# Optimization experiments

Hardware: AMD Instinct MI355X
Metric: run time of the kernel (lower is better)

## Reference

```python
import jax, jax.numpy as jnp
import numpy as np

N, E = 10000, 160000          # nodes, edges
MUL = 128                     # channel multiplicity of 0e and 1o blocks
NSP = 10                      # node_attrs (species one-hot) dim
NRAD = 8                      # edge_feats radial basis dim
SILU_C = 1.6790               # e3nn normalize2mom constant for SiLU
AVG_NEIGH = 16.0
SQ3 = np.sqrt(3.0).astype(np.float32)


def setup_inputs() -> dict:
    key = jax.random.key(0)
    ks = jax.random.split(key, 14)
    d = {}
    d["node_feats"] = jax.random.normal(ks[0], (N, 4 * MUL), jnp.float32)   # [N, 128 + 128*3]
    d["node_attrs"] = jax.random.normal(ks[1], (N, NSP), jnp.float32)
    d["edge_feats"] = jax.random.normal(ks[2], (E, NRAD), jnp.float32)
    d["edge_attrs"] = jax.random.normal(ks[3], (E, 4), jnp.float32)          # [0e | 1o]
    d["edge_index"] = jax.random.randint(ks[4], (2, E), 0, N, jnp.int32)
    # e3nn internal weights are standard normal; normalization applied in forward
    d["lin1_ws"] = jax.random.normal(ks[5], (MUL, MUL), jnp.float32)
    d["lin1_wv"] = jax.random.normal(ks[6], (MUL, MUL), jnp.float32)
    d["fc_w0"] = jax.random.normal(ks[7], (NRAD, 64), jnp.float32)
    d["fc_w1"] = jax.random.normal(ks[8], (64, 64), jnp.float32)
    d["fc_w2"] = jax.random.normal(ks[9], (64, 4 * MUL), jnp.float32)        # tp.weight_numel = 512
    d["lin2_ws"] = jax.random.normal(ks[10], (2 * MUL, MUL), jnp.float32)    # 256x0e -> 128x0e
    d["lin2_wv"] = jax.random.normal(ks[11], (2 * MUL, MUL), jnp.float32)    # 256x1o -> 128x1o
    d["sc_ws"] = jax.random.normal(ks[12], (MUL, NSP, MUL), jnp.float32)
    d["sc_wv"] = jax.random.normal(ks[13], (MUL, NSP, MUL), jnp.float32)
    return d


def _fc(ef, w0, w1, w2):
    # e3nn FullyConnectedNet: x @ W / sqrt(fan_in), normalize2mom-scaled SiLU between layers
    h = SILU_C * jax.nn.silu(ef @ w0 / np.float32(np.sqrt(NRAD)))
    h = SILU_C * jax.nn.silu(h @ w1 / np.float32(8.0))
    return h @ w2 / np.float32(8.0)


def reference(node_feats, node_attrs, edge_feats, edge_attrs, edge_index,
              lin1_ws, lin1_wv, fc_w0, fc_w1, fc_w2,
              lin2_ws, lin2_wv, sc_ws, sc_wv):
    x_s = node_feats[:, :MUL]                       # [N, 128] scalar block
    x_v = node_feats[:, MUL:].reshape(N, MUL, 3)    # [N, 128, 3] vector block

    # self-connection: FullyConnectedTensorProduct with 10x0e attrs; path weight 1/sqrt(mul1*mul2)
    sc_norm = np.float32(1.0 / np.sqrt(MUL * NSP))
    sc_s = jnp.einsum('nu,nv,uvw->nw', x_s, node_attrs, sc_ws) * sc_norm
    sc_v = jnp.einsum('nuc,nv,uvw->nwc', x_v, node_attrs, sc_wv) * sc_norm

    # linear_1 (per-irrep channel mixing, fan_in = 128)
    l1 = np.float32(1.0 / np.sqrt(MUL))
    y_s = (x_s @ lin1_ws) * l1
    y_v = jnp.einsum('nuc,uw->nwc', x_v, lin1_wv) * l1

    src = edge_index[1]
    dst = edge_index[0]
    xs_e = y_s[src]                                 # [E, 128]
    xv_e = y_v[src]                                 # [E, 128, 3]
    a_s = edge_attrs[:, :1]                         # [E, 1]
    a_v = edge_attrs[:, 1:]                         # [E, 3]

    w = _fc(edge_feats, fc_w0, fc_w1, fc_w2)        # [E, 512]
    w_ss, w_sv, w_vs, w_vv = jnp.split(w, 4, axis=1)  # instruction order in source

    # 'uvu' weighted tensor product with e3nn component/element normalization:
    # net coefficient per path works out to 1 except 1o x 1o -> 0e which is 1/sqrt(3)
    mid_s0 = w_ss * xs_e * a_s                                          # 0e*0e->0e
    mid_s1 = w_vv * jnp.einsum('euc,ec->eu', xv_e, a_v) / SQ3           # 1o*1o->0e
    mid_v2 = (w_sv * xs_e)[:, :, None] * a_v[:, None, :]                # 0e*1o->1o
    mid_v3 = w_vs[:, :, None] * xv_e * a_s[:, :, None]                  # 1o*0e->1o

    inv = np.float32(1.0 / np.sqrt(AVG_NEIGH))
    s = jax.ops.segment_sum(jnp.concatenate([mid_s0, mid_s1], axis=1), dst, num_segments=N) * inv  # [N, 256]
    v = jax.ops.segment_sum(jnp.concatenate([mid_v2, mid_v3], axis=1), dst, num_segments=N) * inv  # [N, 256, 3]

    # linear_2 (fan_in = 256)
    l2 = np.float32(1.0 / np.sqrt(2 * MUL))
    out_s = (s @ lin2_ws) * l2 + sc_s
    out_v = jnp.einsum('nuc,uw->nwc', v, lin2_wv) * l2 + sc_v

    return jnp.concatenate([out_s, out_v.reshape(N, 3 * MUL)], axis=1)   # [N, 512]
```

## Files before the change

### kernel.cpp

```cpp
#include <hip/hip_runtime.h>
#include <hip/hip_bf16.h>
#include <math.h>

#define N_NODES 10000
#define N_EDGES 160000
#define S_BLK 79
#define V_BLK 235

typedef __attribute__((ext_vector_type(8))) short short8x;
typedef __attribute__((ext_vector_type(4))) float floatx4;
typedef __attribute__((ext_vector_type(4))) unsigned int uint4x;
typedef __attribute__((ext_vector_type(2))) unsigned int uint2x;

union S8 { short8x v; unsigned short u[8]; uint4 q; };
union U2 { uint2x v; unsigned short us[4]; };

__device__ __forceinline__ unsigned short f2bf(float x) {
    unsigned int u = __float_as_uint(x);
    return (unsigned short)((u + 0x7fffu + ((u >> 16) & 1u)) >> 16);
}
__device__ __forceinline__ float bf2f(unsigned short u) {
    return __uint_as_float(((unsigned)u) << 16);
}
__device__ __forceinline__ float silu_c(float x) {
    return 1.679f * x / (1.0f + __expf(-x));
}

__global__ __launch_bounds__(256) void pack_all_kernel(
    const float* __restrict__ sc_ws, const float* __restrict__ lin2_ws,
    const float* __restrict__ sc_wv, const float* __restrict__ lin2_wv,
    const float* __restrict__ fc_w2, const float* __restrict__ fc_w1,
    const float* __restrict__ lin1_ws, const float* __restrict__ lin1_wv,
    unsigned short* __restrict__ b_pre, unsigned short* __restrict__ w2a,
    unsigned short* __restrict__ w1a, unsigned short* __restrict__ b_lin)
{
    const int bid = blockIdx.x;
    const int t = threadIdx.x;
    if (bid < 192) {
        int id = bid * 256 + t;
        int mat = id / 24576;
        int slot = id - mat * 24576;
        int ks = slot >> 9;
        int rr = slot & 511;
        int lane = rr & 63;
        int quad = lane >> 4;
        int n = ((rr >> 6) << 4) + (lane & 15);
        const float* sc  = mat ? sc_wv  : sc_ws;
        const float* lin = mat ? lin2_wv : lin2_ws;
        S8 pk;
        #pragma unroll
        for (int j = 0; j < 8; j++) {
            int k = ks * 32 + quad * 8 + j;
            float w;
            if (k < 1280) {
                int u = k & 127, v = k >> 7;
                w = sc[(u * 10 + v) * 128 + n];
            } else {
                w = lin[(k - 1280) * 128 + n];
            }
            pk.u[j] = f2bf(w);
        }
        *(uint4*)(b_pre + (size_t)id * 8) = pk.q;
    } else if (bid < 208) {
        int id = (bid - 192) * 256 + t;
        int lane = id & 63;
        int mfg = (id >> 6) & 31;
        int ks = id >> 11;
        int col = mfg * 16 + (lane & 15);
        int k0 = ks * 32 + (lane >> 4) * 8;
        S8 pk;
        #pragma unroll
        for (int j = 0; j < 8; j++)
            pk.u[j] = f2bf(fc_w2[(k0 + j) * 512 + col] * 0.125f);
        *(uint4*)(w2a + (size_t)id * 8) = pk.q;
    } else if (bid < 210) {
        int id = (bid - 208) * 256 + t;
        int lane = id & 63;
        int mf = (id >> 6) & 3;
        int ks = id >> 8;
        int m = mf * 16 + (lane & 15);
        int k0 = ks * 32 + (lane >> 4) * 8;
        S8 pk;
        #pragma unroll
        for (int j = 0; j < 8; j++)
            pk.u[j] = f2bf(fc_w1[(k0 + j) * 64 + m] * 0.125f);
        *(uint4*)(w1a + (size_t)id * 8) = pk.q;
    } else {
        int id = (bid - 210) * 256 + t;
        int mat = id >> 11;
        int slot = id & 2047;
        int ks = slot >> 9;
        int rr = slot & 511;
        int nf = rr >> 6;
        int lane = rr & 63;
        int n = nf * 16 + (lane & 15);
        int k0 = ks * 32 + (lane >> 4) * 8;
        const float* w = mat ? lin1_wv : lin1_ws;
        const float l1 = 0.0883883476483f;
        S8 pk;
        #pragma unroll
        for (int j = 0; j < 8; j++)
            pk.u[j] = f2bf(w[(k0 + j) * 128 + n] * l1);
        *(uint4*)(b_lin + (size_t)id * 8) = pk.q;
    }
}

__global__ __launch_bounds__(256) void node_lin1_mfma(
    const float* __restrict__ node_feats,
    const unsigned short* __restrict__ b_lin,
    unsigned short* __restrict__ y_pk,
    unsigned short* __restrict__ xvP16)
{
    __shared__ __align__(16) unsigned char smem[32768];
    short8x* Al = (short8x*)smem;
    unsigned short* Yt = (unsigned short*)smem;

    const int blk = blockIdx.x;
    const int t = threadIdx.x;
    const int base = blk * 32;
    const int lane = t & 63;
    const int wv = t >> 6;
    const int m15 = lane & 15;
    const int k0q = (lane >> 4) * 8;

    #pragma unroll
    for (int it = 0; it < 8; it++) {
        int g = wv * 8 + it;
        int af = g >> 2;
        int ks = g & 3;
        int m = af * 16 + m15;
        int comp = m >> 5;
        int nloc = m & 31;
        int node = base + nloc;
        int valid = (node < N_NODES);
        if (!valid) node = N_NODES - 1;
        int k0 = ks * 32 + k0q;
        const float* row = node_feats + (size_t)node * 512;
        S8 pk;
        if (comp == 0) {
            float4 a = *(const float4*)&row[k0];
            float4 b = *(const float4*)&row[k0 + 4];
            pk.u[0] = f2bf(a.x); pk.u[1] = f2bf(a.y); pk.u[2] = f2bf(a.z); pk.u[3] = f2bf(a.w);
            pk.u[4] = f2bf(b.x); pk.u[5] = f2bf(b.y); pk.u[6] = f2bf(b.z); pk.u[7] = f2bf(b.w);
        } else {
            int c = comp - 1;
            #pragma unroll
            for (int j = 0; j < 8; j++)
                pk.u[j] = f2bf(row[128 + (k0 + j) * 3 + c]);
            if (valid)
                *(uint4*)&xvP16[((size_t)node * 3 + c) * 128 + k0] = pk.q;
        }
        Al[(ks * 8 + af) * 64 + lane] = pk.v;
    }
    __syncthreads();

    floatx4 c[8][2];
    #pragma unroll
    for (int af = 0; af < 8; af++) {
        c[af][0] = (floatx4){0.f, 0.f, 0.f, 0.f};
        c[af][1] = (floatx4){0.f, 0.f, 0.f, 0.f};
    }

    const uint4* bq = (const uint4*)b_lin;
    #pragma unroll
    for (int ks = 0; ks < 4; ks++) {
        S8 bs0, bs1, bv0, bv1;
        bs0.q = bq[       ks*512 + (wv*2+0)*64 + lane];
        bs1.q = bq[       ks*512 + (wv*2+1)*64 + lane];
        bv0.q = bq[2048 + ks*512 + (wv*2+0)*64 + lane];
        bv1.q = bq[2048 + ks*512 + (wv*2+1)*64 + lane];
        #pragma unroll
        for (int af = 0; af < 8; af++) {
            short8x a = Al[(ks*8 + af)*64 + lane];
            if (af < 2) {
                c[af][0] = __builtin_amdgcn_mfma_f32_16x16x32_bf16(a, bs0.v, c[af][0], 0, 0, 0);
                c[af][1] = __builtin_amdgcn_mfma_f32_16x16x32_bf16(a, bs1.v, c[af][1], 0, 0, 0);
            } else {
                c[af][0] = __builtin_amdgcn_mfma_f32_16x16x32_bf16(a, bv0.v, c[af][0], 0, 0, 0);
                c[af][1] = __builtin_amdgcn_mfma_f32_16x16x32_bf16(a, bv1.v, c[af][1], 0, 0, 0);
            }
        }
    }
    __syncthreads();

    {
        const int rq = (lane >> 4) * 4;
        #pragma unroll
        for (int af = 0; af < 8; af++) {
            #pragma unroll
            for (int nf = 0; nf < 2; nf++) {
                int u = wv * 32 + nf * 16 + m15;
                #pragma unroll
                for (int i = 0; i < 4; i++) {
                    int m = af * 16 + rq + i;
                    int comp = m >> 5, nloc = m & 31;
                    Yt[(nloc * 128 + u) * 4 + comp] = f2bf(c[af][nf][i]);
                }
            }
        }
    }
    __syncthreads();
    {
        unsigned short* dst = y_pk + (size_t)base * 512;
        int nrem = N_NODES - base;
        #pragma unroll
        for (int it = 0; it < 8; it++) {
            int idx = it * 256 + t;
            if ((idx >> 6) < nrem)
                *(uint4*)(dst + (size_t)idx * 8) = *(const uint4*)&Yt[idx * 8];
        }
    }
}

__global__ __launch_bounds__(256) void hist_kernel(const int* __restrict__ edge_index,
                                                   int* __restrict__ deg) {
    int e = blockIdx.x * 256 + threadIdx.x;
    if (e < N_EDGES) atomicAdd(&deg[edge_index[e]], 1);
}

__global__ __launch_bounds__(1024) void scan_kernel(const int* __restrict__ deg,
                                                    int* __restrict__ row_start,
                                                    int* __restrict__ cursor) {
    __shared__ int wsum[16];
    __shared__ int carry_s;
    const int t = threadIdx.x;
    const int lane = t & 63, w = t >> 6;
    if (t == 0) carry_s = 0;
    __syncthreads();
    for (int chunk = 0; chunk < 10; chunk++) {
        int idx = chunk * 1024 + t;
        int v = (idx < N_NODES) ? deg[idx] : 0;
        int x = v;
        #pragma unroll
        for (int off = 1; off < 64; off <<= 1) {
            int yv = __shfl_up(x, off, 64);
            if (lane >= off) x += yv;
        }
        if (lane == 63) wsum[w] = x;
        __syncthreads();
        int wpre = 0;
        for (int i = 0; i < w; i++) wpre += wsum[i];
        int incl = x + wpre + carry_s;
        int excl = incl - v;
        if (idx < N_NODES) { row_start[idx] = excl; cursor[idx] = excl; }
        __syncthreads();
        if (t == 1023) carry_s = incl;
        __syncthreads();
    }
    if (t == 0) row_start[N_NODES] = carry_s;
}

__global__ __launch_bounds__(256) void scatter_kernel(const int* __restrict__ edge_index,
                                                      const float* __restrict__ edge_attrs,
                                                      int* __restrict__ cursor,
                                                      int* __restrict__ edge_list,
                                                      int* __restrict__ srcs,
                                                      float* __restrict__ ea_sorted) {
    int e = blockIdx.x * 256 + threadIdx.x;
    if (e < N_EDGES) {
        int pos = atomicAdd(&cursor[edge_index[e]], 1);
        edge_list[pos] = e;
        srcs[pos] = edge_index[N_EDGES + e];
        float4 ea = *(const float4*)(edge_attrs + (size_t)e * 4);
        *(float4*)(ea_sorted + (size_t)pos * 4) = ea;
    }
}

__global__ __launch_bounds__(256) void edge_w_mfma(
    const float* __restrict__ edge_feats,
    const int* __restrict__ edge_list,
    const float* __restrict__ fc_w0,
    const unsigned short* __restrict__ w1a,
    const unsigned short* __restrict__ w2a,
    unsigned short* __restrict__ w_pk)
{
    __shared__ __align__(16) unsigned char smem[26368];
    float* ef = (float*)smem;
    unsigned short* h0b = (unsigned short*)(smem + 2304);
    unsigned short* T   = (unsigned short*)smem;
    unsigned short* h1b = (unsigned short*)(smem + 16896);
    int* eids = (int*)(smem + 26112);

    const int blk = blockIdx.x;
    const int t = threadIdx.x;
    const int eb0 = blk * 64;
    const int lane = t & 63;
    const int wv = t >> 6;
    const int quad = lane >> 4;
    const int m15 = lane & 15;

    if (t < 64) eids[t] = edge_list[eb0 + t];
    __syncthreads();

    #pragma unroll
    for (int r = 0; r < 2; r++) {
        int idx = r * 256 + t;
        int el = idx >> 3;
        int k = idx & 7;
        ef[el * 9 + k] = edge_feats[(size_t)eids[el] * 8 + k];
    }
    __syncthreads();

    {
        const int e_loc = t >> 2;
        const int c0 = (t & 3) * 16;
        float a0[16];
        #pragma unroll
        for (int i = 0; i < 16; i++) a0[i] = 0.f;
        const float* efr = &ef[e_loc * 9];
        #pragma unroll
        for (int k = 0; k < 8; k++) {
            float ek = efr[k];
            float w[16];
            #pragma unroll
            for (int q4 = 0; q4 < 4; q4++)
                *(float4*)&w[q4*4] = *(const float4*)&fc_w0[k*64 + c0 + q4*4];
            #pragma unroll
            for (int i = 0; i < 16; i++) a0[i] += ek * w[i];
        }
        const float is8 = 0.35355339059f;
        S8 p0, p1;
        #pragma unroll
        for (int i = 0; i < 8; i++) {
            p0.u[i] = f2bf(silu_c(a0[i] * is8));
            p1.u[i] = f2bf(silu_c(a0[8 + i] * is8));
        }
        *(uint4*)&h0b[e_loc * 72 + c0]     = p0.q;
        *(uint4*)&h0b[e_loc * 72 + c0 + 8] = p1.q;
    }
    __syncthreads();

    {
        floatx4 c2[4];
        #pragma unroll
        for (int ee = 0; ee < 4; ee++) c2[ee] = (floatx4){0.f, 0.f, 0.f, 0.f};
        const uint4* w1aq = (const uint4*)w1a;
        #pragma unroll
        for (int ks = 0; ks < 2; ks++) {
            S8 afr;
            afr.q = w1aq[(ks*4 + wv)*64 + lane];
            #pragma unroll
            for (int ee = 0; ee < 4; ee++) {
                S8 bfr;
                bfr.q = *(const uint4*)&h0b[(ee*16 + m15) * 72 + ks*32 + quad*8];
                c2[ee] = __builtin_amdgcn_mfma_f32_16x16x32_bf16(afr.v, bfr.v, c2[ee], 0, 0, 0);
            }
        }
        #pragma unroll
        for (int ee = 0; ee < 4; ee++) {
            ushort4 pk = make_ushort4(f2bf(silu_c(c2[ee][0])), f2bf(silu_c(c2[ee][1])),
                                      f2bf(silu_c(c2[ee][2])), f2bf(silu_c(c2[ee][3])));
            *(ushort4*)&h1b[(ee*16 + m15) * 72 + wv*16 + quad*4] = pk;
        }
    }
    __syncthreads();

    const uint4* w2aq = (const uint4*)w2a;
    #pragma unroll 1
    for (int p = 0; p < 4; p++) {
        floatx4 c3[2][4];
        #pragma unroll
        for (int mf = 0; mf < 2; mf++)
            #pragma unroll
            for (int ee = 0; ee < 4; ee++)
                c3[mf][ee] = (floatx4){0.f, 0.f, 0.f, 0.f};

        #pragma unroll
        for (int ks = 0; ks < 2; ks++) {
            S8 bfr[4];
            #pragma unroll
            for (int ee = 0; ee < 4; ee++)
                bfr[ee].q = *(const uint4*)&h1b[(ee*16 + m15) * 72 + ks*32 + quad*8];
            #pragma unroll
            for (int mf = 0; mf < 2; mf++) {
                S8 afr;
                afr.q = w2aq[(size_t)(ks*32 + wv*8 + p*2 + mf) * 64 + lane];
                #pragma unroll
                for (int ee = 0; ee < 4; ee++)
                    c3[mf][ee] = __builtin_amdgcn_mfma_f32_16x16x32_bf16(afr.v, bfr[ee].v, c3[mf][ee], 0, 0, 0);
            }
        }

        __syncthreads();
        #pragma unroll
        for (int mf = 0; mf < 2; mf++) {
            #pragma unroll
            for (int ee = 0; ee < 4; ee++) {
                int e = ee*16 + m15;
                #pragma unroll
                for (int i = 0; i < 4; i++) {
                    int colp = mf*16 + quad*4 + i;
                    T[e*132 + colp*4 + wv] = f2bf(c3[mf][ee][i]);
                }
            }
        }
        __syncthreads();

        #pragma unroll
        for (int it = 0; it < 8; it++) {
            int idx = it * 256 + t;
            int e  = idx >> 5;
            int cu = idx & 31;
            uint2x v = *(const uint2x*)&T[e*132 + cu*4];
            unsigned short* dstp = w_pk + ((size_t)(eb0 + e) * 128 + p*32 + cu) * 4;
            __builtin_nontemporal_store(v, (uint2x*)dstp);
        }
    }
}

__global__ __launch_bounds__(256) void gather_kernel(
    const int* __restrict__ row_start,
    const int* __restrict__ srcs,
    const float* __restrict__ ea_sorted,
    const unsigned short* __restrict__ w_pk,
    const unsigned short* __restrict__ y_pk,
    float* __restrict__ accS,
    float* __restrict__ accV)
{
    __shared__ float sm[2][128][9];
    const int t = threadIdx.x;
    const int h = t >> 7;
    const int u = t & 127;
    const int n = blockIdx.x;
    const int sbeg = row_start[n];
    const int send = row_start[n + 1];

    float aS0 = 0.f, aS1 = 0.f;
    float aV2x = 0.f, aV2y = 0.f, aV2z = 0.f;
    float aV3x = 0.f, aV3y = 0.f, aV3z = 0.f;

    if (sbeg < send) {
        const int last = send - 1;
        const int i0 = sbeg + h;

        int j0 = (i0     < send) ? i0     : last;
        int j1 = (i0 + 2 < send) ? i0 + 2 : last;
        int s0 = srcs[j0];
        int s1 = srcs[j1];

        U2 wqA, wqB; ushort4 yqA, yqB; float4 eaA, eaB;
        wqA.v = __builtin_nontemporal_load((const uint2x*)(w_pk + ((size_t)j0 * 128 + u) * 4));
        eaA   = *(const float4*)(ea_sorted + (size_t)j0 * 4);
        yqA   = *(const ushort4*)(y_pk + ((size_t)s0 * 128 + u) * 4);
        wqB.v = __builtin_nontemporal_load((const uint2x*)(w_pk + ((size_t)j1 * 128 + u) * 4));
        eaB   = *(const float4*)(ea_sorted + (size_t)j1 * 4);
        yqB   = *(const ushort4*)(y_pk + ((size_t)s1 * 128 + u) * 4);

        int sP0 = srcs[(i0 + 4 < send) ? i0 + 4 : last];
        int sP1 = srcs[(i0 + 6 < send) ? i0 + 6 : last];

        for (int i = i0; i < send; i += 4) {
            {
                float wss = bf2f(wqA.us[0]), wsv = bf2f(wqA.us[1]);
                float wvs = bf2f(wqA.us[2]), wvv = bf2f(wqA.us[3]);
                float qs = bf2f(yqA.x), q0 = bf2f(yqA.y), q1 = bf2f(yqA.z), q2 = bf2f(yqA.w);
                aS0 += wss * qs * eaA.x;
                aS1 += wvv * (q0*eaA.y + q1*eaA.z + q2*eaA.w);
                float tsv = wsv * qs;
                aV2x += tsv * eaA.y; aV2y += tsv * eaA.z; aV2z += tsv * eaA.w;
                float tvs = wvs * eaA.x;
                aV3x += tvs * q0; aV3y += tvs * q1; aV3z += tvs * q2;
            }
            {
                int jn = (i + 4 < send) ? i + 4 : last;
                wqA.v = __builtin_nontemporal_load((const uint2x*)(w_pk + ((size_t)jn * 128 + u) * 4));
                eaA   = *(const float4*)(ea_sorted + (size_t)jn * 4);
                yqA   = *(const ushort4*)(y_pk + ((size_t)sP0 * 128 + u) * 4);
                sP0 = srcs[(i + 8 < send) ? i + 8 : last];
            }
            {
                float m = (i + 2 < send) ? 1.f : 0.f;
                float ex = eaB.x * m, ey = eaB.y * m, ez = eaB.z * m, ew = eaB.w * m;
                float wss = bf2f(wqB.us[0]), wsv = bf2f(wqB.us[1]);
                float wvs = bf2f(wqB.us[2]), wvv = bf2f(wqB.us[3]);
                float qs = bf2f(yqB.x), q0 = bf2f(yqB.y), q1 = bf2f(yqB.z), q2 = bf2f(yqB.w);
                aS0 += wss * qs * ex;
                aS1 += wvv * (q0*ey + q1*ez + q2*ew);
                float tsv = wsv * qs;
                aV2x += tsv * ey; aV2y += tsv * ez; aV2z += tsv * ew;
                float tvs = wvs * ex;
                aV3x += tvs * q0; aV3y += tvs * q1; aV3z += tvs * q2;
            }
            {
                int jn = (i + 6 < send) ? i + 6 : last;
                wqB.v = __builtin_nontemporal_load((const uint2x*)(w_pk + ((size_t)jn * 128 + u) * 4));
                eaB   = *(const float4*)(ea_sorted + (size_t)jn * 4);
                yqB   = *(const ushort4*)(y_pk + ((size_t)sP1 * 128 + u) * 4);
                sP1 = srcs[(i + 10 < send) ? i + 10 : last];
            }
        }
    }

    sm[h][u][0] = aS0;  sm[h][u][1] = aS1;
    sm[h][u][2] = aV2x; sm[h][u][3] = aV2y;
    sm[h][u][4] = aV2z; sm[h][u][5] = aV3x;
    sm[h][u][6] = aV3y; sm[h][u][7] = aV3z;
    __syncthreads();

    const float inv = 0.25f;
    const float s1c = 0.57735026919f * 0.25f;
    if (h == 0) {
        float v0 = sm[0][u][0] + sm[1][u][0];
        float v1 = sm[0][u][1] + sm[1][u][1];
        float v2 = sm[0][u][2] + sm[1][u][2];
        float v3 = sm[0][u][3] + sm[1][u][3];
        accS[(size_t)n * 256 + u]       = v0 * inv;
        accS[(size_t)n * 256 + 128 + u] = v1 * s1c;
        accV[((size_t)n * 3 + 0) * 256 + u] = v2 * inv;
        accV[((size_t)n * 3 + 1) * 256 + u] = v3 * inv;
    } else {
        float v4 = sm[0][u][4] + sm[1][u][4];
        float v5 = sm[0][u][5] + sm[1][u][5];
        float v6 = sm[0][u][6] + sm[1][u][6];
        float v7 = sm[0][u][7] + sm[1][u][7];
        accV[((size_t)n * 3 + 2) * 256 + u]       = v4 * inv;
        accV[((size_t)n * 3 + 0) * 256 + 128 + u] = v5 * inv;
        accV[((size_t)n * 3 + 1) * 256 + 128 + u] = v6 * inv;
        accV[((size_t)n * 3 + 2) * 256 + 128 + u] = v7 * inv;
    }
}

__global__ __launch_bounds__(256) void node_out_mfma(
    const float* __restrict__ node_feats,
    const float* __restrict__ node_attrs,
    const unsigned short* __restrict__ xvP16,
    const float* __restrict__ accS,
    const float* __restrict__ accV,
    const unsigned short* __restrict__ b_pre,
    float* __restrict__ out)
{
    __shared__ short8x Al[512];
    const int bid = blockIdx.x;
    const int t = threadIdx.x;
    const int lane = t & 63;
    const int wv = t >> 6;
    const bool is_s = (bid < S_BLK);

    const int r0g = t >> 2;
    const int q = t & 3;
    const float* pxA[2];
    const unsigned short* pxvA[2];
    const float* paA[2];
    const float* patA[2];
    #pragma unroll
    for (int j = 0; j < 2; j++) {
        int r = r0g + j * 64;
        if (is_s) {
            int R = bid * 128 + r;
            int node = (R < N_NODES) ? R : 0;
            pxA[j]  = node_feats + (size_t)node * 512;
            pxvA[j] = nullptr;
            paA[j]  = accS + (size_t)node * 256;
            patA[j] = node_attrs + node * 10;
        } else {
            int Rg = (bid - S_BLK) * 128 + r;
            if (Rg >= 3 * N_NODES) Rg = 0;
            int node = Rg / 3;
            pxA[j]  = nullptr;
            pxvA[j] = xvP16 + (size_t)Rg * 128;
            paA[j]  = accV + (size_t)Rg * 256;
            patA[j] = node_attrs + node * 10;
        }
    }
    int aslot[2];
    #pragma unroll
    for (int j = 0; j < 2; j++) {
        int r = r0g + j * 64;
        aslot[j] = ((r >> 4) << 6) + (q << 4) + (r & 15);
    }

    const uint4* bfrag_base = (const uint4*)(b_pre) + (is_s ? 0 : 24576);
    const float sc_norm = 0.02795084972f;
    const float l2 = 0.0625f;

    floatx4 c[8][2];
    #pragma unroll
    for (int af = 0; af < 8; af++) {
        c[af][0] = (floatx4){0.f, 0.f, 0.f, 0.f};
        c[af][1] = (floatx4){0.f, 0.f, 0.f, 0.f};
    }

    for (int ks = 0; ks < 48; ks++) {
        S8 b0, b1;
        b0.q = bfrag_base[ks*512 + (wv*2+0)*64 + lane];
        b1.q = bfrag_base[ks*512 + (wv*2+1)*64 + lane];

        __syncthreads();
        {
            int k0 = ks * 32 + q * 8;
            #pragma unroll
            for (int j = 0; j < 2; j++) {
                S8 pk;
                if (k0 < 1280) {
                    int u0 = k0 & 127;
                    float att = patA[j][k0 >> 7] * sc_norm;
                    if (is_s) {
                        #pragma unroll
                        for (int i = 0; i < 8; i++)
                            pk.u[i] = f2bf(pxA[j][u0 + i] * att);
                    } else {
                        #pragma unroll
                        for (int i = 0; i < 8; i++)
                            pk.u[i] = f2bf(bf2f(pxvA[j][u0 + i]) * att);
                    }
                } else {
                    int j2 = k0 - 1280;
                    #pragma unroll
                    for (int i = 0; i < 8; i++)
                        pk.u[i] = f2bf(paA[j][j2 + i] * l2);
                }
                Al[aslot[j]] = pk.v;
            }
        }
        __syncthreads();

        #pragma unroll
        for (int af = 0; af < 8; af++) {
            short8x a = Al[af*64 + lane];
            c[af][0] = __builtin_amdgcn_mfma_f32_16x16x32_bf16(a, b0.v, c[af][0], 0, 0, 0);
            c[af][1] = __builtin_amdgcn_mfma_f32_16x16x32_bf16(a, b1.v, c[af][1], 0, 0, 0);
        }
    }

    const int m = lane & 15;
    const int rq = (lane >> 4) * 4;
    if (is_s) {
        const int n0 = bid * 128;
        #pragma unroll
        for (int af = 0; af < 8; af++) {
            #pragma unroll
            for (int i = 0; i < 4; i++) {
                int n = n0 + af*16 + rq + i;
                if (n < N_NODES) {
                    out[(size_t)n*512 + wv*32 + m]      = c[af][0][i];
                    out[(size_t)n*512 + wv*32 + 16 + m] = c[af][1][i];
                }
            }
        }
    } else {
        const int r0 = (bid - S_BLK) * 128;
        #pragma unroll
        for (int af = 0; af < 8; af++) {
            #pragma unroll
            for (int i = 0; i < 4; i++) {
                int Rg = r0 + af*16 + rq + i;
                if (Rg < 3 * N_NODES) {
                    int nn = Rg / 3;
                    int cc = Rg - nn * 3;
                    float* po = out + (size_t)nn*512 + 128 + cc;
                    po[(wv*32 + m)*3]      = c[af][0][i];
                    po[(wv*32 + 16 + m)*3] = c[af][1][i];
                }
            }
        }
    }
}

extern "C" void kernel_launch(void* const* d_in, const int* in_sizes, int n_in,
                              void* d_out, int out_size, void* d_ws, size_t ws_size,
                              hipStream_t stream) {
    const float* node_feats = (const float*)d_in[0];
    const float* node_attrs = (const float*)d_in[1];
    const float* edge_feats = (const float*)d_in[2];
    const float* edge_attrs = (const float*)d_in[3];
    const int*   edge_index = (const int*)  d_in[4];
    const float* lin1_ws    = (const float*)d_in[5];
    const float* lin1_wv    = (const float*)d_in[6];
    const float* fc_w0      = (const float*)d_in[7];
    const float* fc_w1      = (const float*)d_in[8];
    const float* fc_w2      = (const float*)d_in[9];
    const float* lin2_ws    = (const float*)d_in[10];
    const float* lin2_wv    = (const float*)d_in[11];
    const float* sc_ws      = (const float*)d_in[12];
    const float* sc_wv      = (const float*)d_in[13];
    float* out = (float*)d_out;

    unsigned short* y_pk  = (unsigned short*)d_ws;
    float* accS = (float*)(y_pk + (size_t)5120000);
    float* accV = accS + (size_t)2560000;
    unsigned short* xvP16 = (unsigned short*)(accV + (size_t)7680000);
    unsigned short* w_pk  = xvP16 + (size_t)3840000;
    int* deg       = (int*)(w_pk + (size_t)81920000);
    int* row_start = deg + 10016;
    int* cursor    = row_start + 10016;
    int* edge_list = cursor + 10016;
    int* srcs      = edge_list + N_EDGES;
    float* ea_sorted = (float*)(srcs + N_EDGES);
    unsigned short* b_pre = (unsigned short*)(ea_sorted + (size_t)N_EDGES * 4);
    unsigned short* w2a   = b_pre + (size_t)2 * 24576 * 8;
    unsigned short* w1a   = w2a + (size_t)4096 * 8;
    unsigned short* b_lin = w1a + (size_t)512 * 8;
    const size_t need = (size_t)5120000 * 2 + (size_t)(2560000 + 7680000) * 4
                      + (size_t)3840000 * 2 + (size_t)81920000 * 2
                      + (size_t)(10016 * 3 + N_EDGES * 2) * 4
                      + (size_t)N_EDGES * 4 * 4
                      + ((size_t)2 * 24576 * 8 + (size_t)4096 * 8 + (size_t)512 * 8
                         + (size_t)4096 * 8) * 2;
    if (ws_size < need) return;

    hipLaunchKernelGGL(pack_all_kernel, dim3(226), dim3(256), 0, stream,
                       sc_ws, lin2_ws, sc_wv, lin2_wv, fc_w2, fc_w1, lin1_ws, lin1_wv,
                       b_pre, w2a, w1a, b_lin);
    hipLaunchKernelGGL(node_lin1_mfma, dim3(313), dim3(256), 0, stream,
                       node_feats, b_lin, y_pk, xvP16);

    hipMemsetAsync(deg, 0, (size_t)N_NODES * sizeof(int), stream);
    hipLaunchKernelGGL(hist_kernel, dim3(625), dim3(256), 0, stream, edge_index, deg);
    hipLaunchKernelGGL(scan_kernel, dim3(1), dim3(1024), 0, stream, deg, row_start, cursor);
    hipLaunchKernelGGL(scatter_kernel, dim3(625), dim3(256), 0, stream,
                       edge_index, edge_attrs, cursor, edge_list, srcs, ea_sorted);
    hipLaunchKernelGGL(edge_w_mfma, dim3(2500), dim3(256), 0, stream,
                       edge_feats, edge_list, fc_w0, w1a, w2a, w_pk);
    hipLaunchKernelGGL(gather_kernel, dim3(N_NODES), dim3(256), 0, stream,
                       row_start, srcs, ea_sorted, w_pk, y_pk, accS, accV);

    hipLaunchKernelGGL(node_out_mfma, dim3(S_BLK + V_BLK), dim3(256), 0, stream,
                       node_feats, node_attrs, xvP16, accS, accV, b_pre, out);
}
```

Before: 320.6 us.

## Pipeline node_out_mfma with double-buffered LDS and 64-row tiles

The final node-output GEMM kernel moves from 128-row to 64-row tiles, which doubles the block count. It keeps each row's input features in registers, reusing them across the 10 species slices. A two-slot LDS buffer lets each step pack the next A tile while the MFMAs run on the current one, so one barrier per k-step replaces two. B fragments are prefetched two steps ahead, the accumulator loads are issued early, and s_setprio raises priority during the MFMA bursts. In exchange, B fragments are loaded twice as often per output row and the fully unrolled schedule uses more registers.

```diff
diff --git a/kernel.cpp b/kernel.cpp
--- a/kernel.cpp
+++ b/kernel.cpp
@@ -4,8 +4,8 @@
 
 #define N_NODES 10000
 #define N_EDGES 160000
-#define S_BLK 79
-#define V_BLK 235
+#define SO_BLK 157
+#define VO_BLK 469
 
 typedef __attribute__((ext_vector_type(8))) short short8x;
 typedef __attribute__((ext_vector_type(4))) float floatx4;
@@ -529,118 +529,166 @@
     const unsigned short* __restrict__ b_pre,
     float* __restrict__ out)
 {
-    __shared__ short8x Al[512];
+    __shared__ __align__(16) short8x Abuf[2][256];
     const int bid = blockIdx.x;
     const int t = threadIdx.x;
     const int lane = t & 63;
     const int wv = t >> 6;
-    const bool is_s = (bid < S_BLK);
-
-    const int r0g = t >> 2;
-    const int q = t & 3;
-    const float* pxA[2];
-    const unsigned short* pxvA[2];
-    const float* paA[2];
-    const float* patA[2];
-    #pragma unroll
-    for (int j = 0; j < 2; j++) {
-        int r = r0g + j * 64;
-        if (is_s) {
-            int R = bid * 128 + r;
-            int node = (R < N_NODES) ? R : 0;
-            pxA[j]  = node_feats + (size_t)node * 512;
-            pxvA[j] = nullptr;
-            paA[j]  = accS + (size_t)node * 256;
-            patA[j] = node_attrs + node * 10;
-        } else {
-            int Rg = (bid - S_BLK) * 128 + r;
-            if (Rg >= 3 * N_NODES) Rg = 0;
-            int node = Rg / 3;
-            pxA[j]  = nullptr;
-            pxvA[j] = xvP16 + (size_t)Rg * 128;
-            paA[j]  = accV + (size_t)Rg * 256;
-            patA[j] = node_attrs + node * 10;
-        }
-    }
-    int aslot[2];
-    #pragma unroll
-    for (int j = 0; j < 2; j++) {
-        int r = r0g + j * 64;
-        aslot[j] = ((r >> 4) << 6) + (q << 4) + (r & 15);
-    }
-
-    const uint4* bfrag_base = (const uint4*)(b_pre) + (is_s ? 0 : 24576);
+    const bool is_s = (bid < SO_BLK);
+
+    const int r    = ((t >> 6) << 4) + (t & 15);
+    const int q8   = ((t >> 4) & 3) * 8;
+
+    const float* px = nullptr;
+    const unsigned short* pxv = nullptr;
+    const float* pa;
+    const float* pat;
+    if (is_s) {
+        int R = bid * 64 + r;
+        int node = (R < N_NODES) ? R : 0;
+        px  = node_feats + (size_t)node * 512;
+        pa  = accS + (size_t)node * 256;
+        pat = node_attrs + node * 10;
+    } else {
+        int Rg = (bid - SO_BLK) * 64 + r;
+        if (Rg >= 3 * N_NODES) Rg = 0;
+        int node = Rg / 3;
+        pxv = xvP16 + (size_t)Rg * 128;
+        pa  = accV + (size_t)Rg * 256;
+        pat = node_attrs + node * 10;
+    }
+
+    const uint4* bb = (const uint4*)(b_pre) + (is_s ? 0 : 24576);
     const float sc_norm = 0.02795084972f;
     const float l2 = 0.0625f;
 
-    floatx4 c[8][2];
+    float xf[4][8];
+    S8    xh[4];
+    if (is_s) {
+        #pragma unroll
+        for (int c = 0; c < 4; c++) {
+            floatx4 lo = *(const floatx4*)&px[c*32 + q8];
+            floatx4 hi = *(const floatx4*)&px[c*32 + q8 + 4];
+            #pragma unroll
+            for (int i = 0; i < 4; i++) { xf[c][i] = lo[i]; xf[c][4+i] = hi[i]; }
+        }
+    } else {
+        #pragma unroll
+        for (int c = 0; c < 4; c++)
+            xh[c].q = *(const uint4*)&pxv[c*32 + q8];
+    }
+    float attC = pat[0] * sc_norm;
+
+    floatx4 acc[4][2];
     #pragma unroll
-    for (int af = 0; af < 8; af++) {
-        c[af][0] = (floatx4){0.f, 0.f, 0.f, 0.f};
-        c[af][1] = (floatx4){0.f, 0.f, 0.f, 0.f};
-    }
-
-    for (int ks = 0; ks < 48; ks++) {
-        S8 b0, b1;
-        b0.q = bfrag_base[ks*512 + (wv*2+0)*64 + lane];
-        b1.q = bfrag_base[ks*512 + (wv*2+1)*64 + lane];
-
-        __syncthreads();
-        {
-            int k0 = ks * 32 + q * 8;
-            #pragma unroll
-            for (int j = 0; j < 2; j++) {
-                S8 pk;
-                if (k0 < 1280) {
-                    int u0 = k0 & 127;
-                    float att = patA[j][k0 >> 7] * sc_norm;
-                    if (is_s) {
-                        #pragma unroll
-                        for (int i = 0; i < 8; i++)
-                            pk.u[i] = f2bf(pxA[j][u0 + i] * att);
-                    } else {
-                        #pragma unroll
-                        for (int i = 0; i < 8; i++)
-                            pk.u[i] = f2bf(bf2f(pxvA[j][u0 + i]) * att);
-                    }
-                } else {
-                    int j2 = k0 - 1280;
-                    #pragma unroll
-                    for (int i = 0; i < 8; i++)
-                        pk.u[i] = f2bf(paA[j][j2 + i] * l2);
-                }
-                Al[aslot[j]] = pk.v;
-            }
-        }
-        __syncthreads();
-
-        #pragma unroll
-        for (int af = 0; af < 8; af++) {
-            short8x a = Al[af*64 + lane];
-            c[af][0] = __builtin_amdgcn_mfma_f32_16x16x32_bf16(a, b0.v, c[af][0], 0, 0, 0);
-            c[af][1] = __builtin_amdgcn_mfma_f32_16x16x32_bf16(a, b1.v, c[af][1], 0, 0, 0);
-        }
-    }
+    for (int af = 0; af < 4; af++) {
+        acc[af][0] = (floatx4){0.f, 0.f, 0.f, 0.f};
+        acc[af][1] = (floatx4){0.f, 0.f, 0.f, 0.f};
+    }
+
+    const int cof0 = (wv*2+0)*64 + lane;
+    const int cof1 = (wv*2+1)*64 + lane;
+
+    auto packx = [&](int c_, float att_) -> short8x {
+        S8 pk;
+        if (is_s) {
+            #pragma unroll
+            for (int i = 0; i < 8; i++) pk.u[i] = f2bf(xf[c_][i] * att_);
+        } else {
+            #pragma unroll
+            for (int i = 0; i < 8; i++) pk.u[i] = f2bf(bf2f(xh[c_].u[i]) * att_);
+        }
+        return pk.v;
+    };
+    auto mstep = [&](int kb, const S8& b0, const S8& b1) {
+        __builtin_amdgcn_s_setprio(1);
+        #pragma unroll
+        for (int af = 0; af < 4; af++) {
+            short8x a = Abuf[kb][af*64 + lane];
+            acc[af][0] = __builtin_amdgcn_mfma_f32_16x16x32_bf16(a, b0.v, acc[af][0], 0, 0, 0);
+            acc[af][1] = __builtin_amdgcn_mfma_f32_16x16x32_bf16(a, b1.v, acc[af][1], 0, 0, 0);
+        }
+        __builtin_amdgcn_s_setprio(0);
+    };
+    auto bload = [&](int k2, S8& b0, S8& b1) {
+        b0.q = bb[(size_t)k2*512 + cof0];
+        b1.q = bb[(size_t)k2*512 + cof1];
+    };
+    auto barrier_ = [&]() {
+        asm volatile("s_waitcnt lgkmcnt(0)" ::: "memory");
+        __builtin_amdgcn_s_barrier();
+    };
+
+    S8 bA0, bA1, bB0, bB1;
+    bload(0, bA0, bA1);
+    bload(1, bB0, bB1);
+
+    Abuf[0][t] = packx(0, attC);
+    barrier_();
+
+    #pragma unroll 1
+    for (int vb = 0; vb < 9; vb++) {
+        float attN = pat[vb + 1] * sc_norm;
+        const int ksb = vb * 4;
+        Abuf[1][t] = packx(1, attC); mstep(0, bA0, bA1); bload(ksb+2, bA0, bA1); barrier_();
+        Abuf[0][t] = packx(2, attC); mstep(1, bB0, bB1); bload(ksb+3, bB0, bB1); barrier_();
+        Abuf[1][t] = packx(3, attC); mstep(0, bA0, bA1); bload(ksb+4, bA0, bA1); barrier_();
+        Abuf[0][t] = packx(0, attN); mstep(1, bB0, bB1); bload(ksb+5, bB0, bB1); barrier_();
+        attC = attN;
+    }
+
+    floatx4 aT0[2], aT1[2];
+    auto issue0 = [&](int k_) { int j2 = (k_-40)*32 + q8;
+        aT0[0] = *(const floatx4*)&pa[j2]; aT0[1] = *(const floatx4*)&pa[j2+4]; };
+    auto issue1 = [&](int k_) { int j2 = (k_-40)*32 + q8;
+        aT1[0] = *(const floatx4*)&pa[j2]; aT1[1] = *(const floatx4*)&pa[j2+4]; };
+    auto packT = [&](const floatx4* a2) -> short8x {
+        S8 pk;
+        #pragma unroll
+        for (int i = 0; i < 4; i++) { pk.u[i] = f2bf(a2[0][i] * l2); pk.u[4+i] = f2bf(a2[1][i] * l2); }
+        return pk.v;
+    };
+
+    Abuf[1][t] = packx(1, attC); mstep(0, bA0, bA1); bload(38, bA0, bA1); barrier_();
+    Abuf[0][t] = packx(2, attC); mstep(1, bB0, bB1); bload(39, bB0, bB1); barrier_();
+    issue0(40);
+    Abuf[1][t] = packx(3, attC); mstep(0, bA0, bA1); bload(40, bA0, bA1); barrier_();
+    issue1(41);
+    Abuf[0][t] = packT(aT0); mstep(1, bB0, bB1); bload(41, bB0, bB1); barrier_();
+    issue0(42);
+    Abuf[1][t] = packT(aT1); mstep(0, bA0, bA1); bload(42, bA0, bA1); barrier_();
+    issue1(43);
+    Abuf[0][t] = packT(aT0); mstep(1, bB0, bB1); bload(43, bB0, bB1); barrier_();
+    issue0(44);
+    Abuf[1][t] = packT(aT1); mstep(0, bA0, bA1); bload(44, bA0, bA1); barrier_();
+    issue1(45);
+    Abuf[0][t] = packT(aT0); mstep(1, bB0, bB1); bload(45, bB0, bB1); barrier_();
+    issue0(46);
+    Abuf[1][t] = packT(aT1); mstep(0, bA0, bA1); bload(46, bA0, bA1); barrier_();
+    issue1(47);
+    Abuf[0][t] = packT(aT0); mstep(1, bB0, bB1); bload(47, bB0, bB1); barrier_();
+    Abuf[1][t] = packT(aT1); mstep(0, bA0, bA1); barrier_();
+    mstep(1, bB0, bB1);
 
     const int m = lane & 15;
     const int rq = (lane >> 4) * 4;
     if (is_s) {
-        const int n0 = bid * 128;
-        #pragma unroll
-        for (int af = 0; af < 8; af++) {
+        const int n0 = bid * 64;
+        #pragma unroll
+        for (int af = 0; af < 4; af++) {
             #pragma unroll
             for (int i = 0; i < 4; i++) {
                 int n = n0 + af*16 + rq + i;
                 if (n < N_NODES) {
-                    out[(size_t)n*512 + wv*32 + m]      = c[af][0][i];
-                    out[(size_t)n*512 + wv*32 + 16 + m] = c[af][1][i];
+                    out[(size_t)n*512 + wv*32 + m]      = acc[af][0][i];
+                    out[(size_t)n*512 + wv*32 + 16 + m] = acc[af][1][i];
                 }
             }
         }
     } else {
-        const int r0 = (bid - S_BLK) * 128;
-        #pragma unroll
-        for (int af = 0; af < 8; af++) {
+        const int r0 = (bid - SO_BLK) * 64;
+        #pragma unroll
+        for (int af = 0; af < 4; af++) {
             #pragma unroll
             for (int i = 0; i < 4; i++) {
                 int Rg = r0 + af*16 + rq + i;
@@ -648,8 +696,8 @@
                     int nn = Rg / 3;
                     int cc = Rg - nn * 3;
                     float* po = out + (size_t)nn*512 + 128 + cc;
-                    po[(wv*32 + m)*3]      = c[af][0][i];
-                    po[(wv*32 + 16 + m)*3] = c[af][1][i];
+                    po[(wv*32 + m)*3]      = acc[af][0][i];
+                    po[(wv*32 + 16 + m)*3] = acc[af][1][i];
                 }
             }
         }
@@ -714,6 +762,6 @@
     hipLaunchKernelGGL(gather_kernel, dim3(N_NODES), dim3(256), 0, stream,
                        row_start, srcs, ea_sorted, w_pk, y_pk, accS, accV);
 
-    hipLaunchKernelGGL(node_out_mfma, dim3(S_BLK + V_BLK), dim3(256), 0, stream,
+    hipLaunchKernelGGL(node_out_mfma, dim3(SO_BLK + VO_BLK), dim3(256), 0, stream,
                        node_feats, node_attrs, xvP16, accS, accV, b_pre, out);
 }
```

Result: faster. 289.5 us (-9.7%).
